# Kernel tuning notes

Hardware: AMD Instinct MI355X
Metric: run time of the kernel (lower is better)

Reference implementation:

```python
import jax, jax.numpy as jnp
import numpy as np

N = 100000
E = 1600000
D_IN, D_HID, D_OUT = 128, 256, 128


def setup_inputs() -> dict:
    key = jax.random.key(0)
    ks = jax.random.split(key, 8)
    x = jax.random.normal(ks[0], (N, D_IN), dtype=jnp.float32)
    edge_index = jax.random.randint(ks[1], (2, E), 0, N, dtype=jnp.int64)
    # PyG SAGEConv params: lin_l (applied to aggregated neighbors, has bias),
    # lin_r (applied to root/self, no bias). Stored as [in, out] for x @ W.
    s0 = 1.0 / np.sqrt(D_IN)
    s1 = 1.0 / np.sqrt(D_HID)
    Wl0 = jax.random.uniform(ks[2], (D_IN, D_HID), jnp.float32, -s0, s0)
    bl0 = jnp.zeros((D_HID,), jnp.float32)
    Wr0 = jax.random.uniform(ks[3], (D_IN, D_HID), jnp.float32, -s0, s0)
    Wl1 = jax.random.uniform(ks[4], (D_HID, D_OUT), jnp.float32, -s1, s1)
    bl1 = jnp.zeros((D_OUT,), jnp.float32)
    Wr1 = jax.random.uniform(ks[5], (D_HID, D_OUT), jnp.float32, -s1, s1)
    return {"x": x, "edge_index": edge_index, "Wl0": Wl0, "bl0": bl0,
            "Wr0": Wr0, "Wl1": Wl1, "bl1": bl1, "Wr1": Wr1}


def _sage_conv(x, src, dst, W_l, b_l, W_r, num_nodes):
    # mean-aggregate source features at destination nodes
    msg = x[src]                                         # [E, d] gather
    agg = jax.ops.segment_sum(msg, dst, num_segments=num_nodes)  # [N, d]
    deg = jax.ops.segment_sum(jnp.ones((src.shape[0],), x.dtype), dst,
                              num_segments=num_nodes)    # [N]
    agg = agg / jnp.maximum(deg, 1.0)[:, None]
    return agg @ W_l + b_l + x @ W_r                     # [N, out]


def reference(x, edge_index, Wl0, bl0, Wr0, Wl1, bl1, Wr1):
    src, dst = edge_index[0], edge_index[1]
    n = x.shape[0]
    h = _sage_conv(x, src, dst, Wl0, bl0, Wr0, n)
    h = jax.nn.relu(h)  # dropout is identity in eval mode
    out = _sage_conv(h, src, dst, Wl1, bl1, Wr1, n)
    return out
```

## Files before the change

### kernel.cpp

```cpp
#include <hip/hip_runtime.h>

typedef short bf16x8 __attribute__((ext_vector_type(8)));
typedef float f32x4 __attribute__((ext_vector_type(4)));
typedef unsigned int uint;
typedef unsigned short ushort;
typedef uint u32x2 __attribute__((ext_vector_type(2)));
typedef uint u32x4 __attribute__((ext_vector_type(4)));

#define NBLK 256
#define LCAP 24576
#define HP 264
#define BCAP 6144

__device__ inline ushort f2bf(float f) {
    uint u = __builtin_bit_cast(uint, f);
    uint r = u + 0x7fffu + ((u >> 16) & 1u);
    return (ushort)(r >> 16);
}
__device__ inline float bf2f(uint lo16) {
    uint u = lo16 << 16;
    return __builtin_bit_cast(float, u);
}
__device__ inline float bf2f_hi(uint v) {
    uint u = v & 0xffff0000u;
    return __builtin_bit_cast(float, u);
}

__device__ inline void packw_body(const float* __restrict__ Wa, const float* __restrict__ Wb,
                                  ushort* __restrict__ out, int mode, int tile, int l) {
    int cb = tile >> 3, ks = tile & 7;
    int col = cb * 16 + (l & 15);
    int k0 = ks * 32 + ((l >> 4) * 8);
    ushort vals[8];
#pragma unroll
    for (int j = 0; j < 8; j++) {
        int k = k0 + j;
        float f;
        if (mode == 0)
            f = (k < 128) ? Wa[(size_t)k * 256 + col] : Wb[(size_t)(k - 128) * 256 + col];
        else
            f = (col < 128) ? Wa[(size_t)k * 128 + col] : Wb[(size_t)k * 128 + (col - 128)];
        vals[j] = f2bf(f);
    }
    ushort* dst = out + ((size_t)(ks * 16 + cb) * 64 + l) * 8;
#pragma unroll
    for (int j = 0; j < 8; j++) dst[j] = vals[j];
}

__global__ void prep_kernel(const float* __restrict__ x, ushort* __restrict__ a1,
                            const float* __restrict__ Wr0, const float* __restrict__ Wl0,
                            ushort* __restrict__ w1p,
                            const float* __restrict__ Wl1, const float* __restrict__ Wr1,
                            ushort* __restrict__ w2p,
                            const int* __restrict__ srcv, const int* __restrict__ dstv,
                            int* __restrict__ bcnt, uint* __restrict__ slab,
                            int E, int CE, int NB, int n) {
    __shared__ int hist[512];
    __shared__ int base2[512];
    int bb = blockIdx.x;
    int tid = threadIdx.x;
    if (bb < NBLK) {
        for (int b = tid; b < NB; b += 256) hist[b] = 0;
        __syncthreads();
        int start = bb * CE, end = min(E, start + CE);
        for (int e = start + tid; e < end; e += 256)
            atomicAdd(&hist[dstv[e] >> 8], 1);
        __syncthreads();
        for (int b = tid; b < NB; b += 256) {
            int c = hist[b];
            base2[b] = (c > 0) ? atomicAdd(&bcnt[b], c) : 0;
            hist[b] = 0;
        }
        __syncthreads();
        for (int e = start + tid; e < end; e += 256) {
            int d = dstv[e];
            int s = srcv[e];
            int bkt = d >> 8;
            int off = atomicAdd(&hist[bkt], 1);
            int slot = base2[bkt] + off;
            if (slot < BCAP)
                slab[(size_t)bkt * BCAP + slot] = ((uint)(d & 255) << 17) | (uint)s;
        }
    } else if (bb < NBLK + 64) {
        int r = bb - NBLK;
        int tile = (r & 31) * 4 + (tid >> 6);
        int l = tid & 63;
        if (r < 32) packw_body(Wr0, Wl0, w1p, 0, tile, l);
        else        packw_body(Wl1, Wr1, w2p, 1, tile, l);
    } else {
        int i = (bb - NBLK - 64) * 256 + tid;
        int total = n * 32;
        if (i < total) {
            int row = i >> 5, q = i & 31;
            float4 v = *(const float4*)(x + (size_t)row * 128 + q * 4);
            ushort4 o;
            o.x = f2bf(v.x); o.y = f2bf(v.y); o.z = f2bf(v.z); o.w = f2bf(v.w);
            *(ushort4*)(a1 + (size_t)row * 256 + q * 4) = o;
        }
    }
}

__global__ void pB_kernel(const int* __restrict__ bcnt, int* __restrict__ gbase, int NB) {
    __shared__ int tmp[512];
    int tid = threadIdx.x;
    int v = (tid < NB) ? min(bcnt[tid], BCAP) : 0;
    tmp[tid] = v;
    __syncthreads();
#pragma unroll
    for (int off = 1; off < 512; off <<= 1) {
        int t = (tid >= off) ? tmp[tid - off] : 0;
        __syncthreads();
        tmp[tid] += t;
        __syncthreads();
    }
    if (tid < NB) gbase[tid] = tmp[tid] - v;
}

__global__ void p4_kernel(const uint* __restrict__ slab, const int* __restrict__ bcnt,
                          const int* __restrict__ gbase, int* __restrict__ rs,
                          int* __restrict__ nbr, int n, int E, int NB) {
    __shared__ uint ebuf[LCAP];
    __shared__ int cnt[256];
    __shared__ int cur[256];
    int tid = threadIdx.x;
    int b = blockIdx.x;
    int d0 = b << 8;
    int m = bcnt[b];
    if (m > BCAP) m = BCAP;
    int eb = gbase[b];
    const uint* sl = slab + (size_t)b * BCAP;
    cnt[tid] = 0;
    __syncthreads();
    for (int i = tid; i < m; i += 256) {
        uint v = sl[i];
        if (i < LCAP) ebuf[i] = v;
        atomicAdd(&cnt[v >> 17], 1);
    }
    __syncthreads();
    int v0 = cnt[tid];
    cur[tid] = v0;
    __syncthreads();
#pragma unroll
    for (int off = 1; off < 256; off <<= 1) {
        int t = (tid >= off) ? cur[tid - off] : 0;
        __syncthreads();
        cur[tid] += t;
        __syncthreads();
    }
    int excl = cur[tid] - v0;
    int node = d0 + tid;
    if (node < n) rs[node] = eb + excl;
    if (b == NB - 1 && tid == 0) rs[n] = E;
    __syncthreads();
    cur[tid] = eb + excl;
    __syncthreads();
    for (int i = tid; i < m; i += 256) {
        uint v = (i < LCAP) ? ebuf[i] : sl[i];
        int p = atomicAdd(&cur[v >> 17], 1);
        nbr[p] = (int)(v & 0x1FFFFu);
    }
}

__launch_bounds__(512, 1)
__global__ void fused_gemm_kernel(const ushort* __restrict__ A, const ushort* __restrict__ W1,
                                  const ushort* __restrict__ W2, const float* __restrict__ b0,
                                  const float* __restrict__ b1, ushort* __restrict__ zb,
                                  ushort* __restrict__ sb, int n) {
    extern __shared__ ushort H[];
    int tid = threadIdx.x;
    int l = tid & 63, w = tid >> 6;
    int q = l >> 4, r16 = l & 15;
    int row0 = blockIdx.x * 128;

    {
        int rr = tid >> 5;
        int cc = (tid & 31) * 8;
#pragma unroll
        for (int it = 0; it < 8; it++) {
            int lr = it * 16 + rr;
            int row = row0 + lr;
            if (row > n - 1) row = n - 1;
            u32x4 v = *(const u32x4*)(A + (size_t)row * 256 + cc);
            *(u32x4*)(&H[(size_t)lr * HP + cc]) = v;
        }
    }

    bf16x8 bf1[2][8];
#pragma unroll
    for (int cbi = 0; cbi < 2; cbi++) {
        int cb = 2 * w + cbi;
#pragma unroll
        for (int ks = 0; ks < 8; ks++)
            bf1[cbi][ks] = *(const bf16x8*)(W1 + ((size_t)((ks * 16 + cb) * 64 + l)) * 8);
    }

    f32x4 acc[8][2];
#pragma unroll
    for (int rg = 0; rg < 8; rg++)
#pragma unroll
        for (int cbi = 0; cbi < 2; cbi++) acc[rg][cbi] = (f32x4){0.f, 0.f, 0.f, 0.f};

    __syncthreads();

#pragma unroll
    for (int rg = 0; rg < 8; rg++) {
        bf16x8 a[8];
        const ushort* hp = &H[(size_t)(rg * 16 + r16) * HP + q * 8];
#pragma unroll
        for (int ks = 0; ks < 8; ks++) a[ks] = *(const bf16x8*)(hp + ks * 32);
#pragma unroll
        for (int cbi = 0; cbi < 2; cbi++)
#pragma unroll
            for (int ks = 0; ks < 8; ks++)
                acc[rg][cbi] = __builtin_amdgcn_mfma_f32_16x16x32_bf16(bf1[cbi][ks], a[ks],
                                                                       acc[rg][cbi], 0, 0, 0);
    }

    bf16x8 bf2[2][8];
#pragma unroll
    for (int cbi = 0; cbi < 2; cbi++) {
        int cb = 2 * w + cbi;
#pragma unroll
        for (int ks = 0; ks < 8; ks++)
            bf2[cbi][ks] = *(const bf16x8*)(W2 + ((size_t)((ks * 16 + cb) * 64 + l)) * 8);
    }

    __syncthreads();

#pragma unroll
    for (int rg = 0; rg < 8; rg++) {
#pragma unroll
        for (int cbi = 0; cbi < 2; cbi++) {
            int colb = (2 * w + cbi) * 16 + q * 4;
            f32x4 bv = *(const f32x4*)(b0 + colb);
            f32x4 v = acc[rg][cbi];
            float v0 = fmaxf(v[0] + bv[0], 0.f);
            float v1 = fmaxf(v[1] + bv[1], 0.f);
            float v2 = fmaxf(v[2] + bv[2], 0.f);
            float v3 = fmaxf(v[3] + bv[3], 0.f);
            u32x2 pk;
            pk[0] = (uint)f2bf(v0) | ((uint)f2bf(v1) << 16);
            pk[1] = (uint)f2bf(v2) | ((uint)f2bf(v3) << 16);
            *(u32x2*)(&H[(size_t)(rg * 16 + r16) * HP + colb]) = pk;
            acc[rg][cbi] = (f32x4){0.f, 0.f, 0.f, 0.f};
        }
    }

    __syncthreads();

#pragma unroll
    for (int rg = 0; rg < 8; rg++) {
        bf16x8 a[8];
        const ushort* hp = &H[(size_t)(rg * 16 + r16) * HP + q * 8];
#pragma unroll
        for (int ks = 0; ks < 8; ks++) a[ks] = *(const bf16x8*)(hp + ks * 32);
#pragma unroll
        for (int cbi = 0; cbi < 2; cbi++)
#pragma unroll
            for (int ks = 0; ks < 8; ks++)
                acc[rg][cbi] = __builtin_amdgcn_mfma_f32_16x16x32_bf16(bf2[cbi][ks], a[ks],
                                                                       acc[rg][cbi], 0, 0, 0);
    }

    if (w < 4) {
#pragma unroll
        for (int rg = 0; rg < 8; rg++) {
            int row = row0 + rg * 16 + r16;
#pragma unroll
            for (int cbi = 0; cbi < 2; cbi++) {
                int colb = (2 * w + cbi) * 16 + q * 4;
                f32x4 v = acc[rg][cbi];
                u32x2 pk;
                pk[0] = (uint)f2bf(v[0]) | ((uint)f2bf(v[1]) << 16);
                pk[1] = (uint)f2bf(v[2]) | ((uint)f2bf(v[3]) << 16);
                if (row < n)
                    *(u32x2*)(zb + (size_t)row * 128 + colb) = pk;
            }
        }
    } else {
        int wq = w - 4;
#pragma unroll
        for (int rg = 0; rg < 8; rg++) {
            int row = row0 + rg * 16 + r16;
#pragma unroll
            for (int cbi = 0; cbi < 2; cbi++) {
                int colb = 32 * wq + cbi * 16 + q * 4;
                f32x4 bv = *(const f32x4*)(b1 + colb);
                f32x4 v = acc[rg][cbi];
                v[0] += bv[0]; v[1] += bv[1]; v[2] += bv[2]; v[3] += bv[3];
                u32x2 pk;
                pk[0] = (uint)f2bf(v[0]) | ((uint)f2bf(v[1]) << 16);
                pk[1] = (uint)f2bf(v[2]) | ((uint)f2bf(v[3]) << 16);
                if (row < n)
                    *(u32x2*)(sb + (size_t)row * 128 + colb) = pk;
            }
        }
    }
}

template <int ADD>
__global__ void segmean_kernel(const u32x4* __restrict__ fp, int rstride,
                               const int* __restrict__ rs, const int* __restrict__ nbr,
                               u32x4* __restrict__ outb, int ostride,
                               float* __restrict__ outf, const ushort* __restrict__ sb, int n) {
    int w = threadIdx.x >> 6;
    int l = threadIdx.x & 63;
    int i = blockIdx.x * 4 + w;
    if (i >= n) return;
    int g = l >> 4, f = l & 15;
    int b = rs[i], e = rs[i + 1];
    float a0 = 0.f, a1 = 0.f, a2 = 0.f, a3 = 0.f, a4 = 0.f, a5 = 0.f, a6 = 0.f, a7 = 0.f;
    auto accum = [&](u32x4 v) {
        a0 += bf2f(v[0] & 0xffffu); a1 += bf2f_hi(v[0]);
        a2 += bf2f(v[1] & 0xffffu); a3 += bf2f_hi(v[1]);
        a4 += bf2f(v[2] & 0xffffu); a5 += bf2f_hi(v[2]);
        a6 += bf2f(v[3] & 0xffffu); a7 += bf2f_hi(v[3]);
    };
    int j = b;
    for (; j + 16 <= e; j += 16) {
        int s0 = nbr[j + g], s1 = nbr[j + 4 + g], s2 = nbr[j + 8 + g], s3 = nbr[j + 12 + g];
        u32x4 v0 = fp[(size_t)s0 * rstride + f];
        u32x4 v1 = fp[(size_t)s1 * rstride + f];
        u32x4 v2 = fp[(size_t)s2 * rstride + f];
        u32x4 v3 = fp[(size_t)s3 * rstride + f];
        accum(v0); accum(v1); accum(v2); accum(v3);
    }
    for (; j + 4 <= e; j += 4) {
        u32x4 v = fp[(size_t)nbr[j + g] * rstride + f];
        accum(v);
    }
    int rem = e - j;
    if (g < rem) {
        u32x4 v = fp[(size_t)nbr[j + g] * rstride + f];
        accum(v);
    }
    a0 += __shfl_xor(a0, 32); a0 += __shfl_xor(a0, 16);
    a1 += __shfl_xor(a1, 32); a1 += __shfl_xor(a1, 16);
    a2 += __shfl_xor(a2, 32); a2 += __shfl_xor(a2, 16);
    a3 += __shfl_xor(a3, 32); a3 += __shfl_xor(a3, 16);
    a4 += __shfl_xor(a4, 32); a4 += __shfl_xor(a4, 16);
    a5 += __shfl_xor(a5, 32); a5 += __shfl_xor(a5, 16);
    a6 += __shfl_xor(a6, 32); a6 += __shfl_xor(a6, 16);
    a7 += __shfl_xor(a7, 32); a7 += __shfl_xor(a7, 16);
    if (g == 0) {
        int dg = e - b;
        float inv = 1.0f / (float)(dg > 1 ? dg : 1);
        a0 *= inv; a1 *= inv; a2 *= inv; a3 *= inv;
        a4 *= inv; a5 *= inv; a6 *= inv; a7 *= inv;
        if (ADD) {
            u32x4 sv = *(const u32x4*)(sb + (size_t)i * 128 + f * 8);
            f32x4 o0, o1;
            o0[0] = bf2f(sv[0] & 0xffffu) + a0; o0[1] = bf2f_hi(sv[0]) + a1;
            o0[2] = bf2f(sv[1] & 0xffffu) + a2; o0[3] = bf2f_hi(sv[1]) + a3;
            o1[0] = bf2f(sv[2] & 0xffffu) + a4; o1[1] = bf2f_hi(sv[2]) + a5;
            o1[2] = bf2f(sv[3] & 0xffffu) + a6; o1[3] = bf2f_hi(sv[3]) + a7;
            float* op = outf + (size_t)i * 128 + f * 8;
            *(f32x4*)op = o0;
            *(f32x4*)(op + 4) = o1;
        } else {
            u32x4 pk;
            pk[0] = (uint)f2bf(a0) | ((uint)f2bf(a1) << 16);
            pk[1] = (uint)f2bf(a2) | ((uint)f2bf(a3) << 16);
            pk[2] = (uint)f2bf(a4) | ((uint)f2bf(a5) << 16);
            pk[3] = (uint)f2bf(a6) | ((uint)f2bf(a7) << 16);
            outb[(size_t)i * ostride + f] = pk;
        }
    }
}


extern "C" void kernel_launch(void* const* d_in, const int* in_sizes, int n_in,
                              void* d_out, int out_size, void* d_ws, size_t ws_size,
                              hipStream_t stream) {
    const float* x = (const float*)d_in[0];
    const int* ei = (const int*)d_in[1];
    const float* Wl0 = (const float*)d_in[2];
    const float* bl0 = (const float*)d_in[3];
    const float* Wr0 = (const float*)d_in[4];
    const float* Wl1 = (const float*)d_in[5];
    const float* bl1 = (const float*)d_in[6];
    const float* Wr1 = (const float*)d_in[7];
    float* outp = (float*)d_out;

    int n = in_sizes[0] / 128;
    int E = in_sizes[1] / 2;
    const int* srcv = ei;
    const int* dstv = ei + E;

    int NB = (n + 255) >> 8;
    int CE = (E + NBLK - 1) / NBLK;

    char* w = (char*)d_ws;
    auto align = [](size_t v) { return (v + 255) & ~(size_t)255; };
    size_t off = 0;
    int* rs    = (int*)(w + off); off = align(off + (size_t)(n + 1) * 4);
    int* bcnt  = (int*)(w + off); off = align(off + (size_t)512 * 4);
    int* gbase = (int*)(w + off); off = align(off + (size_t)512 * 4);
    int* nbr   = (int*)(w + off); off = align(off + (size_t)E * 4);
    ushort* a1  = (ushort*)(w + off); off = align(off + (size_t)n * 256 * 2);
    ushort* zb  = (ushort*)(w + off); off = align(off + (size_t)n * 128 * 2);
    ushort* sbf = (ushort*)(w + off); off = align(off + (size_t)n * 128 * 2);
    ushort* w1p = (ushort*)(w + off); off = align(off + (size_t)256 * 256 * 2);
    ushort* w2p = (ushort*)(w + off); off = align(off + (size_t)256 * 256 * 2);
    uint* slab = (uint*)zb;
    (void)ws_size; (void)n_in; (void)out_size;

    int ncx = (n * 32 + 255) / 256;

    hipMemsetAsync(bcnt, 0, (size_t)512 * 4, stream);

    prep_kernel<<<NBLK + 64 + ncx, 256, 0, stream>>>(x, a1, Wr0, Wl0, w1p, Wl1, Wr1, w2p,
                                                     srcv, dstv, bcnt, slab, E, CE, NB, n);
    pB_kernel<<<1, 512, 0, stream>>>(bcnt, gbase, NB);
    p4_kernel<<<NB, 256, 0, stream>>>(slab, bcnt, gbase, rs, nbr, n, E, NB);

    int segb = (n + 3) / 4;
    int mb = (n + 127) / 128;
    int ldsz = 128 * HP * 2;

    hipFuncSetAttribute((const void*)fused_gemm_kernel,
                        hipFuncAttributeMaxDynamicSharedMemorySize, ldsz);

    segmean_kernel<0><<<segb, 256, 0, stream>>>((const u32x4*)a1, 32, rs, nbr,
                                                (u32x4*)a1 + 16, 32, nullptr, nullptr, n);
    fused_gemm_kernel<<<mb, 512, ldsz, stream>>>(a1, w1p, w2p, bl0, bl1, zb, sbf, n);
    segmean_kernel<1><<<segb, 256, 0, stream>>>((const u32x4*)zb, 16, rs, nbr,
                                                nullptr, 0, outp, sbf, n);
}
```

Measured before the change: 250.1 us.

## Fold block-offset scan into p4 and widen fused GEMM to 1024 threads

Removes the separate single-block prefix-scan kernel: each p4 block now sums the counts of all preceding buckets itself with a shared-memory reduction, saving one launch at the cost of redundant reads. The fused GEMM kernel is launched with 16 waves instead of 8, each wave owning one 16-column tile rather than two. This halves per-wave accumulator and weight-fragment registers and gives more waves to hide latency. With launch_bounds(1024,1) the register budget per thread shrinks.

Result: no change. 254.6 us (+1.8%).

```diff
diff --git a/kernel.cpp b/kernel.cpp
--- a/kernel.cpp
+++ b/kernel.cpp
@@ -100,34 +100,26 @@
     }
 }
 
-__global__ void pB_kernel(const int* __restrict__ bcnt, int* __restrict__ gbase, int NB) {
-    __shared__ int tmp[512];
-    int tid = threadIdx.x;
-    int v = (tid < NB) ? min(bcnt[tid], BCAP) : 0;
-    tmp[tid] = v;
-    __syncthreads();
-#pragma unroll
-    for (int off = 1; off < 512; off <<= 1) {
-        int t = (tid >= off) ? tmp[tid - off] : 0;
-        __syncthreads();
-        tmp[tid] += t;
-        __syncthreads();
-    }
-    if (tid < NB) gbase[tid] = tmp[tid] - v;
-}
-
 __global__ void p4_kernel(const uint* __restrict__ slab, const int* __restrict__ bcnt,
-                          const int* __restrict__ gbase, int* __restrict__ rs,
-                          int* __restrict__ nbr, int n, int E, int NB) {
+                          int* __restrict__ rs, int* __restrict__ nbr, int n, int E, int NB) {
     __shared__ uint ebuf[LCAP];
     __shared__ int cnt[256];
     __shared__ int cur[256];
+    __shared__ int red[256];
     int tid = threadIdx.x;
     int b = blockIdx.x;
     int d0 = b << 8;
-    int m = bcnt[b];
-    if (m > BCAP) m = BCAP;
-    int eb = gbase[b];
+    int s = 0;
+    for (int t = tid; t < b; t += 256) s += min(bcnt[t], BCAP);
+    red[tid] = s;
+    __syncthreads();
+#pragma unroll
+    for (int off = 128; off > 0; off >>= 1) {
+        if (tid < off) red[tid] += red[tid + off];
+        __syncthreads();
+    }
+    int eb = red[0];
+    int m = min(bcnt[b], BCAP);
     const uint* sl = slab + (size_t)b * BCAP;
     cnt[tid] = 0;
     __syncthreads();
@@ -161,7 +153,7 @@
     }
 }
 
-__launch_bounds__(512, 1)
+__launch_bounds__(1024, 1)
 __global__ void fused_gemm_kernel(const ushort* __restrict__ A, const ushort* __restrict__ W1,
                                   const ushort* __restrict__ W2, const float* __restrict__ b0,
                                   const float* __restrict__ b1, ushort* __restrict__ zb,
@@ -176,8 +168,8 @@
         int rr = tid >> 5;
         int cc = (tid & 31) * 8;
 #pragma unroll
-        for (int it = 0; it < 8; it++) {
-            int lr = it * 16 + rr;
+        for (int it = 0; it < 4; it++) {
+            int lr = it * 32 + rr;
             int row = row0 + lr;
             if (row > n - 1) row = n - 1;
             u32x4 v = *(const u32x4*)(A + (size_t)row * 256 + cc);
@@ -185,20 +177,14 @@
         }
     }
 
-    bf16x8 bf1[2][8];
-#pragma unroll
-    for (int cbi = 0; cbi < 2; cbi++) {
-        int cb = 2 * w + cbi;
-#pragma unroll
-        for (int ks = 0; ks < 8; ks++)
-            bf1[cbi][ks] = *(const bf16x8*)(W1 + ((size_t)((ks * 16 + cb) * 64 + l)) * 8);
-    }
-
-    f32x4 acc[8][2];
-#pragma unroll
-    for (int rg = 0; rg < 8; rg++)
-#pragma unroll
-        for (int cbi = 0; cbi < 2; cbi++) acc[rg][cbi] = (f32x4){0.f, 0.f, 0.f, 0.f};
+    bf16x8 bf1[8];
+#pragma unroll
+    for (int ks = 0; ks < 8; ks++)
+        bf1[ks] = *(const bf16x8*)(W1 + ((size_t)((ks * 16 + w) * 64 + l)) * 8);
+
+    f32x4 acc[8];
+#pragma unroll
+    for (int rg = 0; rg < 8; rg++) acc[rg] = (f32x4){0.f, 0.f, 0.f, 0.f};
 
     __syncthreads();
 
@@ -209,31 +195,23 @@
 #pragma unroll
         for (int ks = 0; ks < 8; ks++) a[ks] = *(const bf16x8*)(hp + ks * 32);
 #pragma unroll
-        for (int cbi = 0; cbi < 2; cbi++)
-#pragma unroll
-            for (int ks = 0; ks < 8; ks++)
-                acc[rg][cbi] = __builtin_amdgcn_mfma_f32_16x16x32_bf16(bf1[cbi][ks], a[ks],
-                                                                       acc[rg][cbi], 0, 0, 0);
-    }
-
-    bf16x8 bf2[2][8];
-#pragma unroll
-    for (int cbi = 0; cbi < 2; cbi++) {
-        int cb = 2 * w + cbi;
-#pragma unroll
         for (int ks = 0; ks < 8; ks++)
-            bf2[cbi][ks] = *(const bf16x8*)(W2 + ((size_t)((ks * 16 + cb) * 64 + l)) * 8);
-    }
-
-    __syncthreads();
-
-#pragma unroll
-    for (int rg = 0; rg < 8; rg++) {
-#pragma unroll
-        for (int cbi = 0; cbi < 2; cbi++) {
-            int colb = (2 * w + cbi) * 16 + q * 4;
-            f32x4 bv = *(const f32x4*)(b0 + colb);
-            f32x4 v = acc[rg][cbi];
+            acc[rg] = __builtin_amdgcn_mfma_f32_16x16x32_bf16(bf1[ks], a[ks], acc[rg], 0, 0, 0);
+    }
+
+    bf16x8 bf2[8];
+#pragma unroll
+    for (int ks = 0; ks < 8; ks++)
+        bf2[ks] = *(const bf16x8*)(W2 + ((size_t)((ks * 16 + w) * 64 + l)) * 8);
+
+    __syncthreads();
+
+    {
+        int colb = w * 16 + q * 4;
+        f32x4 bv = *(const f32x4*)(b0 + colb);
+#pragma unroll
+        for (int rg = 0; rg < 8; rg++) {
+            f32x4 v = acc[rg];
             float v0 = fmaxf(v[0] + bv[0], 0.f);
             float v1 = fmaxf(v[1] + bv[1], 0.f);
             float v2 = fmaxf(v[2] + bv[2], 0.f);
@@ -242,7 +220,7 @@
             pk[0] = (uint)f2bf(v0) | ((uint)f2bf(v1) << 16);
             pk[1] = (uint)f2bf(v2) | ((uint)f2bf(v3) << 16);
             *(u32x2*)(&H[(size_t)(rg * 16 + r16) * HP + colb]) = pk;
-            acc[rg][cbi] = (f32x4){0.f, 0.f, 0.f, 0.f};
+            acc[rg] = (f32x4){0.f, 0.f, 0.f, 0.f};
         }
     }
 
@@ -255,45 +233,35 @@
 #pragma unroll
         for (int ks = 0; ks < 8; ks++) a[ks] = *(const bf16x8*)(hp + ks * 32);
 #pragma unroll
-        for (int cbi = 0; cbi < 2; cbi++)
-#pragma unroll
-            for (int ks = 0; ks < 8; ks++)
-                acc[rg][cbi] = __builtin_amdgcn_mfma_f32_16x16x32_bf16(bf2[cbi][ks], a[ks],
-                                                                       acc[rg][cbi], 0, 0, 0);
-    }
-
-    if (w < 4) {
+        for (int ks = 0; ks < 8; ks++)
+            acc[rg] = __builtin_amdgcn_mfma_f32_16x16x32_bf16(bf2[ks], a[ks], acc[rg], 0, 0, 0);
+    }
+
+    if (w < 8) {
+        int colb = w * 16 + q * 4;
 #pragma unroll
         for (int rg = 0; rg < 8; rg++) {
             int row = row0 + rg * 16 + r16;
-#pragma unroll
-            for (int cbi = 0; cbi < 2; cbi++) {
-                int colb = (2 * w + cbi) * 16 + q * 4;
-                f32x4 v = acc[rg][cbi];
-                u32x2 pk;
-                pk[0] = (uint)f2bf(v[0]) | ((uint)f2bf(v[1]) << 16);
-                pk[1] = (uint)f2bf(v[2]) | ((uint)f2bf(v[3]) << 16);
-                if (row < n)
-                    *(u32x2*)(zb + (size_t)row * 128 + colb) = pk;
-            }
+            f32x4 v = acc[rg];
+            u32x2 pk;
+            pk[0] = (uint)f2bf(v[0]) | ((uint)f2bf(v[1]) << 16);
+            pk[1] = (uint)f2bf(v[2]) | ((uint)f2bf(v[3]) << 16);
+            if (row < n)
+                *(u32x2*)(zb + (size_t)row * 128 + colb) = pk;
         }
     } else {
-        int wq = w - 4;
+        int colb = (w - 8) * 16 + q * 4;
+        f32x4 bv = *(const f32x4*)(b1 + colb);
 #pragma unroll
         for (int rg = 0; rg < 8; rg++) {
             int row = row0 + rg * 16 + r16;
-#pragma unroll
-            for (int cbi = 0; cbi < 2; cbi++) {
-                int colb = 32 * wq + cbi * 16 + q * 4;
-                f32x4 bv = *(const f32x4*)(b1 + colb);
-                f32x4 v = acc[rg][cbi];
-                v[0] += bv[0]; v[1] += bv[1]; v[2] += bv[2]; v[3] += bv[3];
-                u32x2 pk;
-                pk[0] = (uint)f2bf(v[0]) | ((uint)f2bf(v[1]) << 16);
-                pk[1] = (uint)f2bf(v[2]) | ((uint)f2bf(v[3]) << 16);
-                if (row < n)
-                    *(u32x2*)(sb + (size_t)row * 128 + colb) = pk;
-            }
+            f32x4 v = acc[rg];
+            v[0] += bv[0]; v[1] += bv[1]; v[2] += bv[2]; v[3] += bv[3];
+            u32x2 pk;
+            pk[0] = (uint)f2bf(v[0]) | ((uint)f2bf(v[1]) << 16);
+            pk[1] = (uint)f2bf(v[2]) | ((uint)f2bf(v[3]) << 16);
+            if (row < n)
+                *(u32x2*)(sb + (size_t)row * 128 + colb) = pk;
         }
     }
 }
@@ -395,7 +363,6 @@
     size_t off = 0;
     int* rs    = (int*)(w + off); off = align(off + (size_t)(n + 1) * 4);
     int* bcnt  = (int*)(w + off); off = align(off + (size_t)512 * 4);
-    int* gbase = (int*)(w + off); off = align(off + (size_t)512 * 4);
     int* nbr   = (int*)(w + off); off = align(off + (size_t)E * 4);
     ushort* a1  = (ushort*)(w + off); off = align(off + (size_t)n * 256 * 2);
     ushort* zb  = (ushort*)(w + off); off = align(off + (size_t)n * 128 * 2);
@@ -411,8 +378,7 @@
 
     prep_kernel<<<NBLK + 64 + ncx, 256, 0, stream>>>(x, a1, Wr0, Wl0, w1p, Wl1, Wr1, w2p,
                                                      srcv, dstv, bcnt, slab, E, CE, NB, n);
-    pB_kernel<<<1, 512, 0, stream>>>(bcnt, gbase, NB);
-    p4_kernel<<<NB, 256, 0, stream>>>(slab, bcnt, gbase, rs, nbr, n, E, NB);
+    p4_kernel<<<NB, 256, 0, stream>>>(slab, bcnt, rs, nbr, n, E, NB);
 
     int segb = (n + 3) / 4;
     int mb = (n + 127) / 128;
@@ -423,7 +389,7 @@
 
     segmean_kernel<0><<<segb, 256, 0, stream>>>((const u32x4*)a1, 32, rs, nbr,
                                                 (u32x4*)a1 + 16, 32, nullptr, nullptr, n);
-    fused_gemm_kernel<<<mb, 512, ldsz, stream>>>(a1, w1p, w2p, bl0, bl1, zb, sbf, n);
+    fused_gemm_kernel<<<mb, 1024, ldsz, stream>>>(a1, w1p, w2p, bl0, bl1, zb, sbf, n);
     segmean_kernel<1><<<segb, 256, 0, stream>>>((const u32x4*)zb, 16, rs, nbr,
                                                 nullptr, 0, outp, sbf, n);
 }
```
